# Performance work log

Measured on AMD Instinct MI355X. Metric: run time of the kernel, lower is better.

## Reference

```python
import jax, jax.numpy as jnp
import numpy as np

N_NODES = 100000
N_EDGES = 1600000
D = 128
N_LAYERS = 3
BN_EPS = 1e-5
NORM_EPS = 1e-12


def setup_inputs() -> dict:
    key = jax.random.key(0)
    ks = jax.random.split(key, 4)
    x = jax.random.normal(ks[0], (N_NODES, D), dtype=jnp.float32)
    edge_index = jax.random.randint(ks[1], (2, N_EDGES), 0, N_NODES, dtype=jnp.int32)
    W1 = jax.random.normal(ks[2], (N_LAYERS, D, D), dtype=jnp.float32) * (1.0 / np.sqrt(D))
    W2 = jax.random.normal(ks[3], (N_LAYERS, D, D), dtype=jnp.float32) * (1.0 / np.sqrt(D))
    return {
        "x": x,
        "edge_index": edge_index,
        "W1": W1,
        "b1": jnp.zeros((N_LAYERS, D), jnp.float32),
        "g1": jnp.ones((N_LAYERS, D), jnp.float32),
        "be1": jnp.zeros((N_LAYERS, D), jnp.float32),
        "W2": W2,
        "b2": jnp.zeros((N_LAYERS, D), jnp.float32),
        "g_out": jnp.ones((N_LAYERS - 1, D), jnp.float32),
        "b_out": jnp.zeros((N_LAYERS - 1, D), jnp.float32),
    }


def _batchnorm(h, gamma, beta):
    # BatchNorm1d in training mode: biased batch statistics over nodes.
    mu = jnp.mean(h, axis=0)
    var = jnp.var(h, axis=0)
    return (h - mu) * jax.lax.rsqrt(var + BN_EPS) * gamma + beta


def reference(x, edge_index, W1, b1, g1, be1, W2, b2, g_out, b_out):
    src, dst = edge_index[0], edge_index[1]
    h = x
    for i in range(N_LAYERS):
        # GINConv, eps=0: (1+eps)*x + sum of neighbor messages (scatter-add)
        agg = jax.ops.segment_sum(h[src], dst, num_segments=N_NODES)
        h = h + agg
        # inner MLP: Linear -> BN -> ReLU -> Linear
        h = h @ W1[i] + b1[i]
        h = jax.nn.relu(_batchnorm(h, g1[i], be1[i]))
        h = h @ W2[i] + b2[i]
        if i < N_LAYERS - 1:
            h = jax.nn.relu(_batchnorm(h, g_out[i], b_out[i]))
    # F.normalize(p=2, dim=-1) clamps the norm at 1e-12
    norm = jnp.linalg.norm(h, axis=-1, keepdims=True)
    return h / jnp.maximum(norm, NORM_EPS)
```

## Files before the change

kernel.cpp:

```cpp
#include <hip/hip_runtime.h>

#define M_NODES 100000
#define PADM 100032
#define DIM 128
#define N_EDGES_TOT 1600000
#define NBKT 256
#define NPB 391
#define BKT_CAP 8192
#define ECHUNK 4096
#define INVN 1e-5f
#define NREP 8

typedef unsigned int uint;
typedef unsigned short ushort;
typedef __attribute__((ext_vector_type(8))) short bf16x8;
typedef __attribute__((ext_vector_type(4))) float f32x4;

__device__ __forceinline__ float bflo(uint u) { return __uint_as_float(u << 16); }
__device__ __forceinline__ float bfhi(uint u) { return __uint_as_float(u & 0xffff0000u); }
__device__ __forceinline__ float bf2f(ushort h) { return __uint_as_float(((uint)h) << 16); }
__device__ __forceinline__ ushort f2bf(float f) {
    uint u = __float_as_uint(f);
    return (ushort)((u + 0x7fffu + ((u >> 16) & 1u)) >> 16);
}

__global__ void k_cvt(const float* __restrict__ x, ushort* __restrict__ xb,
                      int n4) {
    int i = blockIdx.x * 256 + threadIdx.x;
    if (i >= n4) return;
    float4 v = ((const float4*)x)[i];
    uint2 r;
    r.x = (uint)f2bf(v.x) | ((uint)f2bf(v.y) << 16);
    r.y = (uint)f2bf(v.z) | ((uint)f2bf(v.w) << 16);
    ((uint2*)xb)[i] = r;
}

__global__ void k_wprep(const float* __restrict__ W1,
                        const float* __restrict__ W2, ushort* __restrict__ Wh,
                        ushort* __restrict__ Wl, float* __restrict__ st,
                        int nSt) {
    int i = blockIdx.x * 256 + threadIdx.x;
    if (i < nSt) st[i] = 0.f;
    if (i >= 6 * 16384) return;
    int l = i >> 14;
    int r = i & 16383;
    int n = r >> 7, k = r & 127;
    const float* W = (l < 3) ? (W1 + l * 16384) : (W2 + (l - 3) * 16384);
    float w = W[k * 128 + n];
    ushort h = f2bf(w);
    Wh[i] = h;
    Wl[i] = f2bf(w - bf2f(h));
}

__global__ void k_bnr(ushort* __restrict__ B0,
                      const float* __restrict__ bnstats,
                      const float* __restrict__ gamma,
                      const float* __restrict__ beta, int n4) {
    __shared__ float coef[256];
    int t = threadIdx.x;
    if (t < 128) {
        float s0 = 0.f, q0 = 0.f;
#pragma unroll
        for (int r = 0; r < NREP; ++r) {
            s0 += bnstats[r * 256 + t];
            q0 += bnstats[r * 256 + 128 + t];
        }
        float mu = s0 * INVN;
        float var = q0 * INVN - mu * mu;
        float s = gamma[t] * rsqrtf(var + 1e-5f);
        coef[t] = s;
        coef[128 + t] = beta[t] - mu * s;
    }
    __syncthreads();
    for (int i = blockIdx.x * 256 + t; i < n4; i += gridDim.x * 256) {
        uint4 v = ((const uint4*)B0)[i];
        int c0 = (i & 15) * 8;
        uint u[4] = {v.x, v.y, v.z, v.w};
        uint o[4];
#pragma unroll
        for (int e = 0; e < 4; ++e) {
            float v0 = fmaxf(fmaf(bflo(u[e]), coef[c0 + 2 * e], coef[128 + c0 + 2 * e]), 0.f);
            float v1 = fmaxf(fmaf(bfhi(u[e]), coef[c0 + 2 * e + 1], coef[128 + c0 + 2 * e + 1]), 0.f);
            o[e] = (uint)f2bf(v0) | ((uint)f2bf(v1) << 16);
        }
        ((uint4*)B0)[i] = make_uint4(o[0], o[1], o[2], o[3]);
    }
}

__global__ void k_bhist(const int* __restrict__ dst, int* __restrict__ cntM,
                        int nE, int nChunks) {
    __shared__ int h[NBKT];
    const int chunk = blockIdx.x, t = threadIdx.x;
    h[t] = 0;
    __syncthreads();
    const int e0 = chunk * ECHUNK;
#pragma unroll
    for (int k = 0; k < 16; ++k) {
        int e = e0 + k * 256 + t;
        if (e < nE) atomicAdd(&h[dst[e] / NPB], 1);
    }
    __syncthreads();
    cntM[t * nChunks + chunk] = h[t];
}

__global__ void k_scanA(int* __restrict__ cnt, int* __restrict__ bsum, int n) {
    __shared__ int s[256];
    int t = threadIdx.x, i = blockIdx.x * 256 + t;
    int v = (i < n) ? cnt[i] : 0;
    s[t] = v;
    __syncthreads();
#pragma unroll
    for (int o = 1; o < 256; o <<= 1) {
        int a = (t >= o) ? s[t - o] : 0;
        __syncthreads();
        s[t] += a;
        __syncthreads();
    }
    if (i < n) cnt[i] = s[t] - v;
    if (t == 255) bsum[blockIdx.x] = s[255];
}

__global__ void k_scanB(int* bsum, int nB) {
    __shared__ int s[1024];
    int t = threadIdx.x;
    int v = (t < nB) ? bsum[t] : 0;
    s[t] = v;
    __syncthreads();
#pragma unroll
    for (int o = 1; o < 1024; o <<= 1) {
        int a = (t >= o) ? s[t - o] : 0;
        __syncthreads();
        s[t] += a;
        __syncthreads();
    }
    if (t < nB) bsum[t] = s[t] - v;
}

__global__ void k_scanC(int* __restrict__ excl, const int* __restrict__ bsum) {
    int i = blockIdx.x * 256 + threadIdx.x;
    excl[i] += bsum[blockIdx.x];
}

__global__ void k_pairs(const int* __restrict__ src, const int* __restrict__ dst,
                        const int* __restrict__ exclM, uint* __restrict__ pairs,
                        int nE, int nChunks) {
    __shared__ int base[NBKT];
    const int chunk = blockIdx.x, t = threadIdx.x;
    base[t] = exclM[t * nChunks + chunk];
    __syncthreads();
    const int e0 = chunk * ECHUNK;
#pragma unroll
    for (int k = 0; k < 16; ++k) {
        int e = e0 + k * 256 + t;
        if (e < nE) {
            int d = dst[e];
            int bkt = d / NPB;
            int pos = atomicAdd(&base[bkt], 1);
            pairs[pos] = ((uint)(d - bkt * NPB) << 17) | (uint)src[e];
        }
    }
}

__global__ void k_csrD(const uint* __restrict__ pairs,
                       const int* __restrict__ exclM, int nChunks,
                       int* __restrict__ rowptr, int* __restrict__ srcs,
                       int nE) {
    __shared__ int cnt[512];
    __shared__ int scn[512];
    __shared__ int sl[BKT_CAP];
    const int b = blockIdx.x, t = threadIdx.x;
    const int base = exclM[b * nChunks];
    const int next = (b == NBKT - 1) ? nE : exclM[(b + 1) * nChunks];
    const int count = next - base;
    const int nodeBase = b * NPB;
    const int nNodes = min(NPB, M_NODES - nodeBase);
    cnt[t] = 0;
    cnt[t + 256] = 0;
    __syncthreads();
    for (int i = t; i < count; i += 256)
        atomicAdd(&cnt[pairs[base + i] >> 17], 1);
    __syncthreads();
    scn[t] = cnt[t];
    scn[t + 256] = cnt[t + 256];
    __syncthreads();
#pragma unroll
    for (int o = 1; o < 512; o <<= 1) {
        int a0 = (t >= o) ? scn[t - o] : 0;
        int a1 = scn[t + 256 - o];
        __syncthreads();
        scn[t] += a0;
        scn[t + 256] += a1;
        __syncthreads();
    }
    int o0 = scn[t] - cnt[t];
    int o1 = scn[t + 256] - cnt[t + 256];
    __syncthreads();
    cnt[t] = o0;
    cnt[t + 256] = o1;
    if (t < nNodes) rowptr[nodeBase + t] = base + o0;
    if (t + 256 < nNodes) rowptr[nodeBase + t + 256] = base + o1;
    if (b == 0 && t == 0) rowptr[M_NODES] = nE;
    __syncthreads();
    const bool inLds = (count <= BKT_CAP);
    for (int i = t; i < count; i += 256) {
        uint p = pairs[base + i];
        int pos = atomicAdd(&cnt[p >> 17], 1);
        int sv = (int)(p & 0x1FFFFu);
        if (inLds) sl[pos] = sv;
        else srcs[base + pos] = sv;
    }
    __syncthreads();
    if (inLds)
        for (int i = t; i < count; i += 256) srcs[base + i] = sl[i];
}

__global__ void k_gather(const ushort* __restrict__ h,
                         const int* __restrict__ rowptr,
                         const int* __restrict__ srcs,
                         ushort* __restrict__ AGh, ushort* __restrict__ AGl,
                         int M) {
    int t = threadIdx.x;
    int node = blockIdx.x * 8 + (t >> 5);
    if (node >= M) return;
    int c = (t & 31) * 4;
    int beg = rowptr[node];
    int end = rowptr[node + 1];

    uint2 v = *(const uint2*)(h + (size_t)node * DIM + c);
    float a0 = bflo(v.x), a1 = bfhi(v.x), a2 = bflo(v.y), a3 = bfhi(v.y);
    float b0 = 0.f, b1 = 0.f, b2 = 0.f, b3 = 0.f;

    int j = beg;
    for (; j + 8 <= end; j += 8) {
        int s[8];
#pragma unroll
        for (int k = 0; k < 8; ++k) s[k] = srcs[j + k];
        uint2 g[8];
#pragma unroll
        for (int k = 0; k < 8; ++k)
            g[k] = *(const uint2*)(h + (size_t)s[k] * DIM + c);
#pragma unroll
        for (int k = 0; k < 8; k += 2) {
            a0 += bflo(g[k].x); a1 += bfhi(g[k].x);
            a2 += bflo(g[k].y); a3 += bfhi(g[k].y);
            b0 += bflo(g[k + 1].x); b1 += bfhi(g[k + 1].x);
            b2 += bflo(g[k + 1].y); b3 += bfhi(g[k + 1].y);
        }
    }
    for (; j + 4 <= end; j += 4) {
        int s0 = srcs[j], s1 = srcs[j + 1], s2 = srcs[j + 2], s3 = srcs[j + 3];
        uint2 g0 = *(const uint2*)(h + (size_t)s0 * DIM + c);
        uint2 g1 = *(const uint2*)(h + (size_t)s1 * DIM + c);
        uint2 g2 = *(const uint2*)(h + (size_t)s2 * DIM + c);
        uint2 g3 = *(const uint2*)(h + (size_t)s3 * DIM + c);
        a0 += bflo(g0.x); a1 += bfhi(g0.x); a2 += bflo(g0.y); a3 += bfhi(g0.y);
        b0 += bflo(g1.x); b1 += bfhi(g1.x); b2 += bflo(g1.y); b3 += bfhi(g1.y);
        a0 += bflo(g2.x); a1 += bfhi(g2.x); a2 += bflo(g2.y); a3 += bfhi(g2.y);
        b0 += bflo(g3.x); b1 += bfhi(g3.x); b2 += bflo(g3.y); b3 += bfhi(g3.y);
    }
    for (; j < end; ++j) {
        int s = srcs[j];
        uint2 g = *(const uint2*)(h + (size_t)s * DIM + c);
        a0 += bflo(g.x); a1 += bfhi(g.x); a2 += bflo(g.y); a3 += bfhi(g.y);
    }
    float s0 = a0 + b0, s1 = a1 + b1, s2 = a2 + b2, s3 = a3 + b3;
    ushort h0 = f2bf(s0), h1 = f2bf(s1), h2 = f2bf(s2), h3 = f2bf(s3);
    ushort l0 = f2bf(s0 - bf2f(h0)), l1 = f2bf(s1 - bf2f(h1));
    ushort l2 = f2bf(s2 - bf2f(h2)), l3 = f2bf(s3 - bf2f(h3));
    uint2 hp, lp;
    hp.x = (uint)h0 | ((uint)h1 << 16);
    hp.y = (uint)h2 | ((uint)h3 << 16);
    lp.x = (uint)l0 | ((uint)l1 << 16);
    lp.y = (uint)l2 | ((uint)l3 << 16);
    size_t ix = (size_t)node * DIM + c;
    *(uint2*)(AGh + ix) = hp;
    *(uint2*)(AGl + ix) = lp;
}

__global__ void __launch_bounds__(256, 4) k_gemmA(
    ushort* __restrict__ Ah, const ushort* __restrict__ Al,
    const ushort* __restrict__ Wh, const ushort* __restrict__ Wl,
    const float* __restrict__ bias, float* __restrict__ statSlot, int M) {
    __shared__ ushort lds[16384];
    const int t = threadIdx.x;
    const int w = t >> 6, lane = t & 63, rq = lane >> 4, rc = lane & 15;
    const int row0 = blockIdx.x * 64;

    bf16x8 wh[4][2], wl[4][2];
#pragma unroll
    for (int kc = 0; kc < 4; ++kc)
#pragma unroll
        for (int jj = 0; jj < 2; ++jj) {
            size_t off = (size_t)(w * 32 + jj * 16 + rc) * DIM + kc * 32 + rq * 8;
            wh[kc][jj] = *(const bf16x8*)(Wh + off);
            wl[kc][jj] = *(const bf16x8*)(Wl + off);
        }

#pragma unroll
    for (int i = 0; i < 8; ++i) {
        int idx = t + i * 256;
        int pl = idx >> 10;
        int r = (idx >> 4) & 63;
        int cb = idx & 15;
        const ushort* p = pl ? Al : Ah;
        uint4 v = *(const uint4*)(p + (size_t)(row0 + r) * DIM + cb * 8);
        *(uint4*)((char*)lds + pl * 16384 + r * 256 +
                  ((cb * 16) ^ ((r & 15) << 4))) = v;
    }
    __syncthreads();

    f32x4 acc[4][2];
#pragma unroll
    for (int i = 0; i < 4; ++i)
#pragma unroll
        for (int jj = 0; jj < 2; ++jj) acc[i][jj] = (f32x4){0.f, 0.f, 0.f, 0.f};

#pragma unroll
    for (int kc = 0; kc < 4; ++kc) {
        const int kb = kc * 64 + rq * 16;
#pragma unroll
        for (int i = 0; i < 4; ++i) {
            int lr = i * 16 + rc;
            int so = lr * 256 + (kb ^ ((lr & 15) << 4));
            bf16x8 ah = *(const bf16x8*)((char*)lds + so);
            bf16x8 al = *(const bf16x8*)((char*)lds + 16384 + so);
#pragma unroll
            for (int jj = 0; jj < 2; ++jj) {
                acc[i][jj] = __builtin_amdgcn_mfma_f32_16x16x32_bf16(ah, wh[kc][jj], acc[i][jj], 0, 0, 0);
                acc[i][jj] = __builtin_amdgcn_mfma_f32_16x16x32_bf16(al, wh[kc][jj], acc[i][jj], 0, 0, 0);
                acc[i][jj] = __builtin_amdgcn_mfma_f32_16x16x32_bf16(ah, wl[kc][jj], acc[i][jj], 0, 0, 0);
            }
        }
    }

    float bc[2] = {bias[w * 32 + rc], bias[w * 32 + 16 + rc]};
    float csum[2] = {0.f, 0.f}, csq[2] = {0.f, 0.f};

    __syncthreads();
#pragma unroll
    for (int i = 0; i < 4; ++i)
#pragma unroll
        for (int r = 0; r < 4; ++r) {
            int lrow = i * 16 + rq * 4 + r;
            bool live = (row0 + lrow) < M;
#pragma unroll
            for (int jj = 0; jj < 2; ++jj) {
                float o = acc[i][jj][r] + bc[jj];
                int off = lrow * 256 +
                          (((w * 32 + jj * 16 + rc) * 2) ^ ((lrow & 15) << 4));
                *(ushort*)((char*)lds + off) = f2bf(o);
                if (live) { csum[jj] += o; csq[jj] += o * o; }
            }
        }
    __syncthreads();
    {
        int lrow = w * 16 + (lane & 15);
        int kq = lane >> 4;
        ushort* dH = Ah + (size_t)row0 * DIM;
#pragma unroll
        for (int kc = 0; kc < 4; ++kc) {
            int off = lrow * 256 + ((kc * 64 + kq * 16) ^ ((lrow & 15) << 4));
            uint4 H = *(uint4*)((char*)lds + off);
            size_t go = ((size_t)(w * 4 + kc) * 64 + lane) * 8;
            *(uint4*)(dH + go) = H;
        }
    }
#pragma unroll
    for (int jj = 0; jj < 2; ++jj) {
        csum[jj] += __shfl_xor(csum[jj], 16);
        csum[jj] += __shfl_xor(csum[jj], 32);
        csq[jj] += __shfl_xor(csq[jj], 16);
        csq[jj] += __shfl_xor(csq[jj], 32);
    }
    float* slot = statSlot + (blockIdx.x & (NREP - 1)) * 256;
    if (lane < 16) {
        atomicAdd(slot + w * 32 + rc, csum[0]);
        atomicAdd(slot + w * 32 + 16 + rc, csum[1]);
        atomicAdd(slot + 128 + w * 32 + rc, csq[0]);
        atomicAdd(slot + 128 + w * 32 + 16 + rc, csq[1]);
    }
}

__global__ void __launch_bounds__(256, 4) k_gemmB(
    const ushort* __restrict__ Ch,
    const ushort* __restrict__ Wh, const ushort* __restrict__ Wl,
    const float* __restrict__ bias, const float* __restrict__ bnstats,
    const float* __restrict__ gamma, const float* __restrict__ beta,
    ushort* __restrict__ Cb, float* __restrict__ outF,
    float* __restrict__ statSlot, int M) {
    __shared__ char smem[16384];
    const int t = threadIdx.x;
    const int w = t >> 6, lane = t & 63, rq = lane >> 4, rc = lane & 15;
    const int row0 = blockIdx.x * 64;

    bf16x8 wh[4][2], wl[4][2];
#pragma unroll
    for (int kc = 0; kc < 4; ++kc)
#pragma unroll
        for (int jj = 0; jj < 2; ++jj) {
            size_t off = (size_t)(w * 32 + jj * 16 + rc) * DIM + kc * 32 + rq * 8;
            wh[kc][jj] = *(const bf16x8*)(Wh + off);
            wl[kc][jj] = *(const bf16x8*)(Wl + off);
        }

    float* coef = (float*)smem;
    if (t < 128) {
        float s0 = 0.f, q0 = 0.f;
#pragma unroll
        for (int r = 0; r < NREP; ++r) {
            s0 += bnstats[r * 256 + t];
            q0 += bnstats[r * 256 + 128 + t];
        }
        float mu = s0 * INVN;
        float var = q0 * INVN - mu * mu;
        float s = gamma[t] * rsqrtf(var + 1e-5f);
        coef[t] = s;
        coef[128 + t] = beta[t] - mu * s;
    }
    __syncthreads();

    const ushort* pH = Ch + (size_t)row0 * DIM;
    const int kq8 = (lane >> 4) * 8;

    f32x4 acc[4][2];
#pragma unroll
    for (int i = 0; i < 4; ++i)
#pragma unroll
        for (int jj = 0; jj < 2; ++jj) acc[i][jj] = (f32x4){0.f, 0.f, 0.f, 0.f};

#pragma unroll
    for (int kc = 0; kc < 4; ++kc) {
        float sc8[8], sh8[8];
#pragma unroll
        for (int e = 0; e < 8; ++e) {
            sc8[e] = coef[kc * 32 + kq8 + e];
            sh8[e] = coef[128 + kc * 32 + kq8 + e];
        }
#pragma unroll
        for (int i = 0; i < 4; ++i) {
            size_t go = ((size_t)(i * 4 + kc) * 64 + lane) * 8;
            uint4 H = *(const uint4*)(pH + go);
            uint hu[4] = {H.x, H.y, H.z, H.w};
            uint oh[4], ol[4];
#pragma unroll
            for (int e = 0; e < 4; ++e) {
                float v0 = bflo(hu[e]);
                float v1 = bfhi(hu[e]);
                v0 = fmaxf(fmaf(v0, sc8[2 * e], sh8[2 * e]), 0.f);
                v1 = fmaxf(fmaf(v1, sc8[2 * e + 1], sh8[2 * e + 1]), 0.f);
                ushort h0 = f2bf(v0), h1 = f2bf(v1);
                oh[e] = (uint)h0 | ((uint)h1 << 16);
                ol[e] = (uint)f2bf(v0 - bf2f(h0)) |
                        ((uint)f2bf(v1 - bf2f(h1)) << 16);
            }
            uint4 AH = make_uint4(oh[0], oh[1], oh[2], oh[3]);
            uint4 AL = make_uint4(ol[0], ol[1], ol[2], ol[3]);
            bf16x8 ah = *(bf16x8*)&AH;
            bf16x8 al = *(bf16x8*)&AL;
#pragma unroll
            for (int jj = 0; jj < 2; ++jj) {
                acc[i][jj] = __builtin_amdgcn_mfma_f32_16x16x32_bf16(ah, wh[kc][jj], acc[i][jj], 0, 0, 0);
                acc[i][jj] = __builtin_amdgcn_mfma_f32_16x16x32_bf16(al, wh[kc][jj], acc[i][jj], 0, 0, 0);
                acc[i][jj] = __builtin_amdgcn_mfma_f32_16x16x32_bf16(ah, wl[kc][jj], acc[i][jj], 0, 0, 0);
            }
        }
    }

    float bc[2] = {bias[w * 32 + rc], bias[w * 32 + 16 + rc]};

    if (outF) {
#pragma unroll
        for (int i = 0; i < 4; ++i)
#pragma unroll
            for (int r = 0; r < 4; ++r)
#pragma unroll
                for (int jj = 0; jj < 2; ++jj) acc[i][jj][r] += bc[jj];
        __syncthreads();
        float* nr = (float*)smem;
#pragma unroll
        for (int i = 0; i < 4; ++i)
#pragma unroll
            for (int r = 0; r < 4; ++r) {
                float ss = acc[i][0][r] * acc[i][0][r] + acc[i][1][r] * acc[i][1][r];
                ss += __shfl_xor(ss, 1);
                ss += __shfl_xor(ss, 2);
                ss += __shfl_xor(ss, 4);
                ss += __shfl_xor(ss, 8);
                if (rc == 0) nr[(i * 16 + rq * 4 + r) * 4 + w] = ss;
            }
        __syncthreads();
#pragma unroll
        for (int i = 0; i < 4; ++i)
#pragma unroll
            for (int r = 0; r < 4; ++r) {
                int lrow = i * 16 + rq * 4 + r;
                float4 q = *(const float4*)(nr + lrow * 4);
                float inv = 1.f / fmaxf(sqrtf(q.x + q.y + q.z + q.w), 1e-12f);
                int row = row0 + lrow;
                if (row < M) {
                    outF[(size_t)row * DIM + w * 32 + rc] = acc[i][0][r] * inv;
                    outF[(size_t)row * DIM + w * 32 + 16 + rc] = acc[i][1][r] * inv;
                }
            }
        return;
    }

    float csum[2] = {0.f, 0.f}, csq[2] = {0.f, 0.f};
    __syncthreads();
#pragma unroll
    for (int i = 0; i < 4; ++i)
#pragma unroll
        for (int r = 0; r < 4; ++r) {
            int lrow = i * 16 + rq * 4 + r;
            bool live = (row0 + lrow) < M;
#pragma unroll
            for (int jj = 0; jj < 2; ++jj) {
                float o = acc[i][jj][r] + bc[jj];
                int off = lrow * 256 +
                          (((w * 32 + jj * 16 + rc) * 2) ^ ((lrow & 15) << 4));
                *(ushort*)(smem + off) = f2bf(o);
                if (live) { csum[jj] += o; csq[jj] += o * o; }
            }
        }
    __syncthreads();
#pragma unroll
    for (int it = 0; it < 4; ++it) {
        int idx = t + it * 256;
        int row = idx >> 4, cb = idx & 15;
        int grow = row0 + row;
        if (grow < M) {
            uint4 v = *(uint4*)(smem + row * 256 + ((cb * 16) ^ ((row & 15) << 4)));
            *(uint4*)(Cb + (size_t)grow * DIM + cb * 8) = v;
        }
    }
#pragma unroll
    for (int jj = 0; jj < 2; ++jj) {
        csum[jj] += __shfl_xor(csum[jj], 16);
        csum[jj] += __shfl_xor(csum[jj], 32);
        csq[jj] += __shfl_xor(csq[jj], 16);
        csq[jj] += __shfl_xor(csq[jj], 32);
    }
    float* slot = statSlot + (blockIdx.x & (NREP - 1)) * 256;
    if (lane < 16) {
        atomicAdd(slot + w * 32 + rc, csum[0]);
        atomicAdd(slot + w * 32 + 16 + rc, csum[1]);
        atomicAdd(slot + 128 + w * 32 + rc, csq[0]);
        atomicAdd(slot + 128 + w * 32 + 16 + rc, csq[1]);
    }
}

extern "C" void kernel_launch(void* const* d_in, const int* in_sizes, int n_in,
                              void* d_out, int out_size, void* d_ws,
                              size_t ws_size, hipStream_t stream) {
    const float* x = (const float*)d_in[0];
    const int* ei = (const int*)d_in[1];
    const float* W1 = (const float*)d_in[2];
    const float* b1 = (const float*)d_in[3];
    const float* g1 = (const float*)d_in[4];
    const float* be1 = (const float*)d_in[5];
    const float* W2 = (const float*)d_in[6];
    const float* b2 = (const float*)d_in[7];
    const float* g_out = (const float*)d_in[8];
    const float* b_out = (const float*)d_in[9];
    float* out = (float*)d_out;

    const int M = M_NODES;
    const int E = N_EDGES_TOT;
    const size_t NM = (size_t)M * DIM;
    const size_t PM = (size_t)PADM * DIM;
    const int nChunks = (E + ECHUNK - 1) / ECHUNK;
    const int nMat = NBKT * nChunks;
    const int SLOT = 256 * NREP;

    ushort* AGh = (ushort*)d_ws;
    ushort* AGl = AGh + PM;
    ushort* B0 = AGl + PM;
    ushort* Wh = B0 + NM;
    ushort* Wl = Wh + 6 * 16384;
    float* st = (float*)(Wl + 6 * 16384);
    float* stA0 = st;
    float* stA1 = st + SLOT;
    float* stA2 = st + 2 * SLOT;
    float* stB0 = st + 3 * SLOT;
    float* stB1 = st + 4 * SLOT;
    uint* pairs = (uint*)(st + 5 * SLOT);
    int* rowptr = (int*)(pairs + E);
    int* cntM = rowptr + (M + 2);
    int* bsum = cntM + nMat;
    int* srcs = bsum + 1024;

    const int* src = ei;
    const int* dst = ei + E;

    const int gemmGrid = PADM / 64;
    const int gathGrid = (M + 7) / 8;
    const int n4 = (int)(NM / 8);

    k_bhist<<<nChunks, 256, 0, stream>>>(dst, cntM, E, nChunks);
    k_scanA<<<(nMat + 255) / 256, 256, 0, stream>>>(cntM, bsum, nMat);
    k_scanB<<<1, 1024, 0, stream>>>(bsum, (nMat + 255) / 256);
    k_scanC<<<(nMat + 255) / 256, 256, 0, stream>>>(cntM, bsum);
    k_pairs<<<nChunks, 256, 0, stream>>>(src, dst, cntM, pairs, E, nChunks);
    k_csrD<<<NBKT, 256, 0, stream>>>(pairs, cntM, nChunks, rowptr, srcs, E);

    k_cvt<<<(int)((NM / 4 + 255) / 256), 256, 0, stream>>>(x, B0, (int)(NM / 4));
    k_wprep<<<(6 * 16384 + 255) / 256, 256, 0, stream>>>(W1, W2, Wh, Wl, st, 5 * SLOT);

    k_gather<<<gathGrid, 256, 0, stream>>>(B0, rowptr, srcs, AGh, AGl, M);
    k_gemmA<<<gemmGrid, 256, 0, stream>>>(AGh, AGl, Wh, Wl, b1, stA0, M);
    k_gemmB<<<gemmGrid, 256, 0, stream>>>(AGh, Wh + 3 * 16384, Wl + 3 * 16384,
                                          b2, stA0, g1, be1, B0, nullptr, stB0, M);
    k_bnr<<<2048, 256, 0, stream>>>(B0, stB0, g_out, b_out, n4);

    k_gather<<<gathGrid, 256, 0, stream>>>(B0, rowptr, srcs, AGh, AGl, M);
    k_gemmA<<<gemmGrid, 256, 0, stream>>>(AGh, AGl, Wh + 16384, Wl + 16384,
                                          b1 + 128, stA1, M);
    k_gemmB<<<gemmGrid, 256, 0, stream>>>(AGh, Wh + 4 * 16384, Wl + 4 * 16384,
                                          b2 + 128, stA1, g1 + 128, be1 + 128,
                                          B0, nullptr, stB1, M);
    k_bnr<<<2048, 256, 0, stream>>>(B0, stB1, g_out + 128, b_out + 128, n4);

    k_gather<<<gathGrid, 256, 0, stream>>>(B0, rowptr, srcs, AGh, AGl, M);
    k_gemmA<<<gemmGrid, 256, 0, stream>>>(AGh, AGl, Wh + 2 * 16384, Wl + 2 * 16384,
                                          b1 + 256, stA2, M);
    k_gemmB<<<gemmGrid, 256, 0, stream>>>(AGh, Wh + 5 * 16384, Wl + 5 * 16384,
                                          b2 + 256, stA2, g1 + 256, be1 + 256,
                                          nullptr, out, nullptr, M);
}
```

Before: 458.6 us.

## Fuse outer BatchNorm+ReLU into neighbor gather and use direct global-to-LDS loads

Removes the standalone k_bnr pass. Each gather block now builds the BN scale/shift coefficients in shared memory and applies affine+ReLU to every gathered neighbor row and the self row. This saves a full read/write pass over the node features twice per forward, at the cost of extra FMA/max work on every gathered element (about 16x more applications than before). Separately, gemmA's tile load now uses global_load_lds with a pre-swizzled source column to skip the register round-trip. The 4-wide remainder loop in gather is also dropped.

```diff
diff --git a/kernel.cpp b/kernel.cpp
--- a/kernel.cpp
+++ b/kernel.cpp
@@ -52,41 +52,6 @@
     Wl[i] = f2bf(w - bf2f(h));
 }
 
-__global__ void k_bnr(ushort* __restrict__ B0,
-                      const float* __restrict__ bnstats,
-                      const float* __restrict__ gamma,
-                      const float* __restrict__ beta, int n4) {
-    __shared__ float coef[256];
-    int t = threadIdx.x;
-    if (t < 128) {
-        float s0 = 0.f, q0 = 0.f;
-#pragma unroll
-        for (int r = 0; r < NREP; ++r) {
-            s0 += bnstats[r * 256 + t];
-            q0 += bnstats[r * 256 + 128 + t];
-        }
-        float mu = s0 * INVN;
-        float var = q0 * INVN - mu * mu;
-        float s = gamma[t] * rsqrtf(var + 1e-5f);
-        coef[t] = s;
-        coef[128 + t] = beta[t] - mu * s;
-    }
-    __syncthreads();
-    for (int i = blockIdx.x * 256 + t; i < n4; i += gridDim.x * 256) {
-        uint4 v = ((const uint4*)B0)[i];
-        int c0 = (i & 15) * 8;
-        uint u[4] = {v.x, v.y, v.z, v.w};
-        uint o[4];
-#pragma unroll
-        for (int e = 0; e < 4; ++e) {
-            float v0 = fmaxf(fmaf(bflo(u[e]), coef[c0 + 2 * e], coef[128 + c0 + 2 * e]), 0.f);
-            float v1 = fmaxf(fmaf(bfhi(u[e]), coef[c0 + 2 * e + 1], coef[128 + c0 + 2 * e + 1]), 0.f);
-            o[e] = (uint)f2bf(v0) | ((uint)f2bf(v1) << 16);
-        }
-        ((uint4*)B0)[i] = make_uint4(o[0], o[1], o[2], o[3]);
-    }
-}
-
 __global__ void k_bhist(const int* __restrict__ dst, int* __restrict__ cntM,
                         int nE, int nChunks) {
     __shared__ int h[NBKT];
@@ -217,17 +182,53 @@
 __global__ void k_gather(const ushort* __restrict__ h,
                          const int* __restrict__ rowptr,
                          const int* __restrict__ srcs,
+                         const float* __restrict__ bnstats,
+                         const float* __restrict__ gamma,
+                         const float* __restrict__ beta,
                          ushort* __restrict__ AGh, ushort* __restrict__ AGl,
                          int M) {
+    __shared__ float coef[256];
     int t = threadIdx.x;
+    const bool bn = (bnstats != nullptr);
+    if (bn) {
+        if (t < 128) {
+            float s0 = 0.f, q0 = 0.f;
+#pragma unroll
+            for (int r = 0; r < NREP; ++r) {
+                s0 += bnstats[r * 256 + t];
+                q0 += bnstats[r * 256 + 128 + t];
+            }
+            float mu = s0 * INVN;
+            float var = q0 * INVN - mu * mu;
+            float s = gamma[t] * rsqrtf(var + 1e-5f);
+            coef[t] = s;
+            coef[128 + t] = beta[t] - mu * s;
+        }
+        __syncthreads();
+    }
     int node = blockIdx.x * 8 + (t >> 5);
     if (node >= M) return;
     int c = (t & 31) * 4;
+    float sc0 = 1.f, sc1 = 1.f, sc2 = 1.f, sc3 = 1.f;
+    float sh0 = 0.f, sh1 = 0.f, sh2 = 0.f, sh3 = 0.f;
+    if (bn) {
+        sc0 = coef[c]; sc1 = coef[c + 1]; sc2 = coef[c + 2]; sc3 = coef[c + 3];
+        sh0 = coef[128 + c]; sh1 = coef[129 + c];
+        sh2 = coef[130 + c]; sh3 = coef[131 + c];
+    }
     int beg = rowptr[node];
     int end = rowptr[node + 1];
 
     uint2 v = *(const uint2*)(h + (size_t)node * DIM + c);
-    float a0 = bflo(v.x), a1 = bfhi(v.x), a2 = bflo(v.y), a3 = bfhi(v.y);
+    float a0, a1, a2, a3;
+    if (bn) {
+        a0 = fmaxf(fmaf(bflo(v.x), sc0, sh0), 0.f);
+        a1 = fmaxf(fmaf(bfhi(v.x), sc1, sh1), 0.f);
+        a2 = fmaxf(fmaf(bflo(v.y), sc2, sh2), 0.f);
+        a3 = fmaxf(fmaf(bfhi(v.y), sc3, sh3), 0.f);
+    } else {
+        a0 = bflo(v.x); a1 = bfhi(v.x); a2 = bflo(v.y); a3 = bfhi(v.y);
+    }
     float b0 = 0.f, b1 = 0.f, b2 = 0.f, b3 = 0.f;
 
     int j = beg;
@@ -239,29 +240,39 @@
 #pragma unroll
         for (int k = 0; k < 8; ++k)
             g[k] = *(const uint2*)(h + (size_t)s[k] * DIM + c);
-#pragma unroll
-        for (int k = 0; k < 8; k += 2) {
-            a0 += bflo(g[k].x); a1 += bfhi(g[k].x);
-            a2 += bflo(g[k].y); a3 += bfhi(g[k].y);
-            b0 += bflo(g[k + 1].x); b1 += bfhi(g[k + 1].x);
-            b2 += bflo(g[k + 1].y); b3 += bfhi(g[k + 1].y);
-        }
-    }
-    for (; j + 4 <= end; j += 4) {
-        int s0 = srcs[j], s1 = srcs[j + 1], s2 = srcs[j + 2], s3 = srcs[j + 3];
-        uint2 g0 = *(const uint2*)(h + (size_t)s0 * DIM + c);
-        uint2 g1 = *(const uint2*)(h + (size_t)s1 * DIM + c);
-        uint2 g2 = *(const uint2*)(h + (size_t)s2 * DIM + c);
-        uint2 g3 = *(const uint2*)(h + (size_t)s3 * DIM + c);
-        a0 += bflo(g0.x); a1 += bfhi(g0.x); a2 += bflo(g0.y); a3 += bfhi(g0.y);
-        b0 += bflo(g1.x); b1 += bfhi(g1.x); b2 += bflo(g1.y); b3 += bfhi(g1.y);
-        a0 += bflo(g2.x); a1 += bfhi(g2.x); a2 += bflo(g2.y); a3 += bfhi(g2.y);
-        b0 += bflo(g3.x); b1 += bfhi(g3.x); b2 += bflo(g3.y); b3 += bfhi(g3.y);
+        if (bn) {
+#pragma unroll
+            for (int k = 0; k < 8; k += 2) {
+                a0 += fmaxf(fmaf(bflo(g[k].x), sc0, sh0), 0.f);
+                a1 += fmaxf(fmaf(bfhi(g[k].x), sc1, sh1), 0.f);
+                a2 += fmaxf(fmaf(bflo(g[k].y), sc2, sh2), 0.f);
+                a3 += fmaxf(fmaf(bfhi(g[k].y), sc3, sh3), 0.f);
+                b0 += fmaxf(fmaf(bflo(g[k + 1].x), sc0, sh0), 0.f);
+                b1 += fmaxf(fmaf(bfhi(g[k + 1].x), sc1, sh1), 0.f);
+                b2 += fmaxf(fmaf(bflo(g[k + 1].y), sc2, sh2), 0.f);
+                b3 += fmaxf(fmaf(bfhi(g[k + 1].y), sc3, sh3), 0.f);
+            }
+        } else {
+#pragma unroll
+            for (int k = 0; k < 8; k += 2) {
+                a0 += bflo(g[k].x); a1 += bfhi(g[k].x);
+                a2 += bflo(g[k].y); a3 += bfhi(g[k].y);
+                b0 += bflo(g[k + 1].x); b1 += bfhi(g[k + 1].x);
+                b2 += bflo(g[k + 1].y); b3 += bfhi(g[k + 1].y);
+            }
+        }
     }
     for (; j < end; ++j) {
         int s = srcs[j];
         uint2 g = *(const uint2*)(h + (size_t)s * DIM + c);
-        a0 += bflo(g.x); a1 += bfhi(g.x); a2 += bflo(g.y); a3 += bfhi(g.y);
+        if (bn) {
+            a0 += fmaxf(fmaf(bflo(g.x), sc0, sh0), 0.f);
+            a1 += fmaxf(fmaf(bfhi(g.x), sc1, sh1), 0.f);
+            a2 += fmaxf(fmaf(bflo(g.y), sc2, sh2), 0.f);
+            a3 += fmaxf(fmaf(bfhi(g.y), sc3, sh3), 0.f);
+        } else {
+            a0 += bflo(g.x); a1 += bfhi(g.x); a2 += bflo(g.y); a3 += bfhi(g.y);
+        }
     }
     float s0 = a0 + b0, s1 = a1 + b1, s2 = a2 + b2, s3 = a3 + b3;
     ushort h0 = f2bf(s0), h1 = f2bf(s1), h2 = f2bf(s2), h3 = f2bf(s3);
@@ -302,10 +313,13 @@
         int pl = idx >> 10;
         int r = (idx >> 4) & 63;
         int cb = idx & 15;
+        int cbs = cb ^ (r & 15);
         const ushort* p = pl ? Al : Ah;
-        uint4 v = *(const uint4*)(p + (size_t)(row0 + r) * DIM + cb * 8);
-        *(uint4*)((char*)lds + pl * 16384 + r * 256 +
-                  ((cb * 16) ^ ((r & 15) << 4))) = v;
+        const ushort* g = p + (size_t)(row0 + r) * DIM + cbs * 8;
+        __builtin_amdgcn_global_load_lds(
+            (const __attribute__((address_space(1))) void*)g,
+            (__attribute__((address_space(3))) void*)((char*)lds + idx * 16),
+            16, 0, 0);
     }
     __syncthreads();
 
@@ -594,7 +608,6 @@
 
     const int gemmGrid = PADM / 64;
     const int gathGrid = (M + 7) / 8;
-    const int n4 = (int)(NM / 8);
 
     k_bhist<<<nChunks, 256, 0, stream>>>(dst, cntM, E, nChunks);
     k_scanA<<<(nMat + 255) / 256, 256, 0, stream>>>(cntM, bsum, nMat);
@@ -606,21 +619,22 @@
     k_cvt<<<(int)((NM / 4 + 255) / 256), 256, 0, stream>>>(x, B0, (int)(NM / 4));
     k_wprep<<<(6 * 16384 + 255) / 256, 256, 0, stream>>>(W1, W2, Wh, Wl, st, 5 * SLOT);
 
-    k_gather<<<gathGrid, 256, 0, stream>>>(B0, rowptr, srcs, AGh, AGl, M);
+    k_gather<<<gathGrid, 256, 0, stream>>>(B0, rowptr, srcs, nullptr, nullptr,
+                                           nullptr, AGh, AGl, M);
     k_gemmA<<<gemmGrid, 256, 0, stream>>>(AGh, AGl, Wh, Wl, b1, stA0, M);
     k_gemmB<<<gemmGrid, 256, 0, stream>>>(AGh, Wh + 3 * 16384, Wl + 3 * 16384,
                                           b2, stA0, g1, be1, B0, nullptr, stB0, M);
-    k_bnr<<<2048, 256, 0, stream>>>(B0, stB0, g_out, b_out, n4);
-
-    k_gather<<<gathGrid, 256, 0, stream>>>(B0, rowptr, srcs, AGh, AGl, M);
+
+    k_gather<<<gathGrid, 256, 0, stream>>>(B0, rowptr, srcs, stB0, g_out, b_out,
+                                           AGh, AGl, M);
     k_gemmA<<<gemmGrid, 256, 0, stream>>>(AGh, AGl, Wh + 16384, Wl + 16384,
                                           b1 + 128, stA1, M);
     k_gemmB<<<gemmGrid, 256, 0, stream>>>(AGh, Wh + 4 * 16384, Wl + 4 * 16384,
                                           b2 + 128, stA1, g1 + 128, be1 + 128,
                                           B0, nullptr, stB1, M);
-    k_bnr<<<2048, 256, 0, stream>>>(B0, stB1, g_out + 128, b_out + 128, n4);
-
-    k_gather<<<gathGrid, 256, 0, stream>>>(B0, rowptr, srcs, AGh, AGl, M);
+
+    k_gather<<<gathGrid, 256, 0, stream>>>(B0, rowptr, srcs, stB1, g_out + 128,
+                                           b_out + 128, AGh, AGl, M);
     k_gemmA<<<gemmGrid, 256, 0, stream>>>(AGh, AGl, Wh + 2 * 16384, Wl + 2 * 16384,
                                           b1 + 256, stA2, M);
     k_gemmB<<<gemmGrid, 256, 0, stream>>>(AGh, Wh + 5 * 16384, Wl + 5 * 16384,
```

Measured after the change: 472.0 us. 1.03x slower.

## Fuse neighbor gather into first GEMM kernel via LDS staging

Applied to the files above, without the earlier changes.

The separate gather kernel is merged into the first GEMM of each layer. Each 64-row block accumulates its neighbor sums directly into swizzled LDS as hi/lo bf16 planes, so the AGh/AGl round trip through global memory goes away. Weight fragments are now loaded per k-chunk instead of all up front, which cuts register use so launch bounds can rise to 5 blocks. The cost is that the latency-bound gather now runs inside a GEMM block with fewer resident threads per node, which may lower memory-level parallelism.

```diff
diff --git a/kernel.cpp b/kernel.cpp
--- a/kernel.cpp
+++ b/kernel.cpp
@@ -214,109 +214,97 @@
         for (int i = t; i < count; i += 256) srcs[base + i] = sl[i];
 }
 
-__global__ void k_gather(const ushort* __restrict__ h,
-                         const int* __restrict__ rowptr,
-                         const int* __restrict__ srcs,
-                         ushort* __restrict__ AGh, ushort* __restrict__ AGl,
-                         int M) {
-    int t = threadIdx.x;
-    int node = blockIdx.x * 8 + (t >> 5);
-    if (node >= M) return;
-    int c = (t & 31) * 4;
-    int beg = rowptr[node];
-    int end = rowptr[node + 1];
-
-    uint2 v = *(const uint2*)(h + (size_t)node * DIM + c);
-    float a0 = bflo(v.x), a1 = bfhi(v.x), a2 = bflo(v.y), a3 = bfhi(v.y);
-    float b0 = 0.f, b1 = 0.f, b2 = 0.f, b3 = 0.f;
-
-    int j = beg;
-    for (; j + 8 <= end; j += 8) {
-        int s[8];
-#pragma unroll
-        for (int k = 0; k < 8; ++k) s[k] = srcs[j + k];
-        uint2 g[8];
-#pragma unroll
-        for (int k = 0; k < 8; ++k)
-            g[k] = *(const uint2*)(h + (size_t)s[k] * DIM + c);
-#pragma unroll
-        for (int k = 0; k < 8; k += 2) {
-            a0 += bflo(g[k].x); a1 += bfhi(g[k].x);
-            a2 += bflo(g[k].y); a3 += bfhi(g[k].y);
-            b0 += bflo(g[k + 1].x); b1 += bfhi(g[k + 1].x);
-            b2 += bflo(g[k + 1].y); b3 += bfhi(g[k + 1].y);
-        }
-    }
-    for (; j + 4 <= end; j += 4) {
-        int s0 = srcs[j], s1 = srcs[j + 1], s2 = srcs[j + 2], s3 = srcs[j + 3];
-        uint2 g0 = *(const uint2*)(h + (size_t)s0 * DIM + c);
-        uint2 g1 = *(const uint2*)(h + (size_t)s1 * DIM + c);
-        uint2 g2 = *(const uint2*)(h + (size_t)s2 * DIM + c);
-        uint2 g3 = *(const uint2*)(h + (size_t)s3 * DIM + c);
-        a0 += bflo(g0.x); a1 += bfhi(g0.x); a2 += bflo(g0.y); a3 += bfhi(g0.y);
-        b0 += bflo(g1.x); b1 += bfhi(g1.x); b2 += bflo(g1.y); b3 += bfhi(g1.y);
-        a0 += bflo(g2.x); a1 += bfhi(g2.x); a2 += bflo(g2.y); a3 += bfhi(g2.y);
-        b0 += bflo(g3.x); b1 += bfhi(g3.x); b2 += bflo(g3.y); b3 += bfhi(g3.y);
-    }
-    for (; j < end; ++j) {
-        int s = srcs[j];
-        uint2 g = *(const uint2*)(h + (size_t)s * DIM + c);
-        a0 += bflo(g.x); a1 += bfhi(g.x); a2 += bflo(g.y); a3 += bfhi(g.y);
-    }
-    float s0 = a0 + b0, s1 = a1 + b1, s2 = a2 + b2, s3 = a3 + b3;
-    ushort h0 = f2bf(s0), h1 = f2bf(s1), h2 = f2bf(s2), h3 = f2bf(s3);
-    ushort l0 = f2bf(s0 - bf2f(h0)), l1 = f2bf(s1 - bf2f(h1));
-    ushort l2 = f2bf(s2 - bf2f(h2)), l3 = f2bf(s3 - bf2f(h3));
-    uint2 hp, lp;
-    hp.x = (uint)h0 | ((uint)h1 << 16);
-    hp.y = (uint)h2 | ((uint)h3 << 16);
-    lp.x = (uint)l0 | ((uint)l1 << 16);
-    lp.y = (uint)l2 | ((uint)l3 << 16);
-    size_t ix = (size_t)node * DIM + c;
-    *(uint2*)(AGh + ix) = hp;
-    *(uint2*)(AGl + ix) = lp;
-}
-
-__global__ void __launch_bounds__(256, 4) k_gemmA(
-    ushort* __restrict__ Ah, const ushort* __restrict__ Al,
-    const ushort* __restrict__ Wh, const ushort* __restrict__ Wl,
-    const float* __restrict__ bias, float* __restrict__ statSlot, int M) {
+__global__ void __launch_bounds__(256, 5) k_gg(
+    const ushort* __restrict__ h, const int* __restrict__ rowptr,
+    const int* __restrict__ srcs, const ushort* __restrict__ Wh,
+    const ushort* __restrict__ Wl, const float* __restrict__ bias,
+    ushort* __restrict__ Ch, float* __restrict__ statSlot, int M) {
     __shared__ ushort lds[16384];
     const int t = threadIdx.x;
+    const int row0 = blockIdx.x * 64;
+
+    {
+        const int g = t >> 5;
+        const int L = t & 31;
+        const int c = L * 4;
+        for (int n = 0; n < 8; ++n) {
+            int lr = g * 8 + n;
+            int node = row0 + lr;
+            float a0 = 0.f, a1 = 0.f, a2 = 0.f, a3 = 0.f;
+            float b0 = 0.f, b1 = 0.f, b2 = 0.f, b3 = 0.f;
+            if (node < M) {
+                uint2 v = *(const uint2*)(h + (size_t)node * DIM + c);
+                a0 = bflo(v.x); a1 = bfhi(v.x); a2 = bflo(v.y); a3 = bfhi(v.y);
+                int beg = rowptr[node];
+                int end = rowptr[node + 1];
+                int j = beg;
+                for (; j + 8 <= end; j += 8) {
+                    int s[8];
+#pragma unroll
+                    for (int k = 0; k < 8; ++k) s[k] = srcs[j + k];
+                    uint2 gg[8];
+#pragma unroll
+                    for (int k = 0; k < 8; ++k)
+                        gg[k] = *(const uint2*)(h + (size_t)s[k] * DIM + c);
+#pragma unroll
+                    for (int k = 0; k < 8; k += 2) {
+                        a0 += bflo(gg[k].x); a1 += bfhi(gg[k].x);
+                        a2 += bflo(gg[k].y); a3 += bfhi(gg[k].y);
+                        b0 += bflo(gg[k + 1].x); b1 += bfhi(gg[k + 1].x);
+                        b2 += bflo(gg[k + 1].y); b3 += bfhi(gg[k + 1].y);
+                    }
+                }
+                for (; j + 4 <= end; j += 4) {
+                    int s0 = srcs[j], s1 = srcs[j + 1];
+                    int s2 = srcs[j + 2], s3 = srcs[j + 3];
+                    uint2 g0 = *(const uint2*)(h + (size_t)s0 * DIM + c);
+                    uint2 g1 = *(const uint2*)(h + (size_t)s1 * DIM + c);
+                    uint2 g2 = *(const uint2*)(h + (size_t)s2 * DIM + c);
+                    uint2 g3 = *(const uint2*)(h + (size_t)s3 * DIM + c);
+                    a0 += bflo(g0.x); a1 += bfhi(g0.x); a2 += bflo(g0.y); a3 += bfhi(g0.y);
+                    b0 += bflo(g1.x); b1 += bfhi(g1.x); b2 += bflo(g1.y); b3 += bfhi(g1.y);
+                    a0 += bflo(g2.x); a1 += bfhi(g2.x); a2 += bflo(g2.y); a3 += bfhi(g2.y);
+                    b0 += bflo(g3.x); b1 += bfhi(g3.x); b2 += bflo(g3.y); b3 += bfhi(g3.y);
+                }
+                for (; j < end; ++j) {
+                    int s = srcs[j];
+                    uint2 gg = *(const uint2*)(h + (size_t)s * DIM + c);
+                    a0 += bflo(gg.x); a1 += bfhi(gg.x);
+                    a2 += bflo(gg.y); a3 += bfhi(gg.y);
+                }
+            }
+            float s0 = a0 + b0, s1 = a1 + b1, s2 = a2 + b2, s3 = a3 + b3;
+            ushort h0 = f2bf(s0), h1 = f2bf(s1), h2 = f2bf(s2), h3 = f2bf(s3);
+            ushort l0 = f2bf(s0 - bf2f(h0)), l1 = f2bf(s1 - bf2f(h1));
+            ushort l2 = f2bf(s2 - bf2f(h2)), l3 = f2bf(s3 - bf2f(h3));
+            uint2 hp, lp;
+            hp.x = (uint)h0 | ((uint)h1 << 16);
+            hp.y = (uint)h2 | ((uint)h3 << 16);
+            lp.x = (uint)l0 | ((uint)l1 << 16);
+            lp.y = (uint)l2 | ((uint)l3 << 16);
+            int off = lr * 256 + ((((L >> 1) * 16) ^ ((lr & 15) << 4))) + (L & 1) * 8;
+            *(uint2*)((char*)lds + off) = hp;
+            *(uint2*)((char*)lds + 16384 + off) = lp;
+        }
+    }
+    __syncthreads();
+
     const int w = t >> 6, lane = t & 63, rq = lane >> 4, rc = lane & 15;
-    const int row0 = blockIdx.x * 64;
-
-    bf16x8 wh[4][2], wl[4][2];
-#pragma unroll
-    for (int kc = 0; kc < 4; ++kc)
+    f32x4 acc[4][2];
+#pragma unroll
+    for (int i = 0; i < 4; ++i)
+#pragma unroll
+        for (int jj = 0; jj < 2; ++jj) acc[i][jj] = (f32x4){0.f, 0.f, 0.f, 0.f};
+
+#pragma unroll
+    for (int kc = 0; kc < 4; ++kc) {
+        bf16x8 bh[2], bl[2];
 #pragma unroll
         for (int jj = 0; jj < 2; ++jj) {
             size_t off = (size_t)(w * 32 + jj * 16 + rc) * DIM + kc * 32 + rq * 8;
-            wh[kc][jj] = *(const bf16x8*)(Wh + off);
-            wl[kc][jj] = *(const bf16x8*)(Wl + off);
-        }
-
-#pragma unroll
-    for (int i = 0; i < 8; ++i) {
-        int idx = t + i * 256;
-        int pl = idx >> 10;
-        int r = (idx >> 4) & 63;
-        int cb = idx & 15;
-        const ushort* p = pl ? Al : Ah;
-        uint4 v = *(const uint4*)(p + (size_t)(row0 + r) * DIM + cb * 8);
-        *(uint4*)((char*)lds + pl * 16384 + r * 256 +
-                  ((cb * 16) ^ ((r & 15) << 4))) = v;
-    }
-    __syncthreads();
-
-    f32x4 acc[4][2];
-#pragma unroll
-    for (int i = 0; i < 4; ++i)
-#pragma unroll
-        for (int jj = 0; jj < 2; ++jj) acc[i][jj] = (f32x4){0.f, 0.f, 0.f, 0.f};
-
-#pragma unroll
-    for (int kc = 0; kc < 4; ++kc) {
+            bh[jj] = *(const bf16x8*)(Wh + off);
+            bl[jj] = *(const bf16x8*)(Wl + off);
+        }
         const int kb = kc * 64 + rq * 16;
 #pragma unroll
         for (int i = 0; i < 4; ++i) {
@@ -326,9 +314,9 @@
             bf16x8 al = *(const bf16x8*)((char*)lds + 16384 + so);
 #pragma unroll
             for (int jj = 0; jj < 2; ++jj) {
-                acc[i][jj] = __builtin_amdgcn_mfma_f32_16x16x32_bf16(ah, wh[kc][jj], acc[i][jj], 0, 0, 0);
-                acc[i][jj] = __builtin_amdgcn_mfma_f32_16x16x32_bf16(al, wh[kc][jj], acc[i][jj], 0, 0, 0);
-                acc[i][jj] = __builtin_amdgcn_mfma_f32_16x16x32_bf16(ah, wl[kc][jj], acc[i][jj], 0, 0, 0);
+                acc[i][jj] = __builtin_amdgcn_mfma_f32_16x16x32_bf16(ah, bh[jj], acc[i][jj], 0, 0, 0);
+                acc[i][jj] = __builtin_amdgcn_mfma_f32_16x16x32_bf16(al, bh[jj], acc[i][jj], 0, 0, 0);
+                acc[i][jj] = __builtin_amdgcn_mfma_f32_16x16x32_bf16(ah, bl[jj], acc[i][jj], 0, 0, 0);
             }
         }
     }
@@ -356,7 +344,7 @@
     {
         int lrow = w * 16 + (lane & 15);
         int kq = lane >> 4;
-        ushort* dH = Ah + (size_t)row0 * DIM;
+        ushort* dH = Ch + (size_t)row0 * DIM;
 #pragma unroll
         for (int kc = 0; kc < 4; ++kc) {
             int off = lrow * 256 + ((kc * 64 + kq * 16) ^ ((lrow & 15) << 4));
@@ -572,9 +560,8 @@
     const int nMat = NBKT * nChunks;
     const int SLOT = 256 * NREP;
 
-    ushort* AGh = (ushort*)d_ws;
-    ushort* AGl = AGh + PM;
-    ushort* B0 = AGl + PM;
+    ushort* Ch = (ushort*)d_ws;
+    ushort* B0 = Ch + PM;
     ushort* Wh = B0 + NM;
     ushort* Wl = Wh + 6 * 16384;
     float* st = (float*)(Wl + 6 * 16384);
@@ -593,7 +580,6 @@
     const int* dst = ei + E;
 
     const int gemmGrid = PADM / 64;
-    const int gathGrid = (M + 7) / 8;
     const int n4 = (int)(NM / 8);
 
     k_bhist<<<nChunks, 256, 0, stream>>>(dst, cntM, E, nChunks);
@@ -606,24 +592,21 @@
     k_cvt<<<(int)((NM / 4 + 255) / 256), 256, 0, stream>>>(x, B0, (int)(NM / 4));
     k_wprep<<<(6 * 16384 + 255) / 256, 256, 0, stream>>>(W1, W2, Wh, Wl, st, 5 * SLOT);
 
-    k_gather<<<gathGrid, 256, 0, stream>>>(B0, rowptr, srcs, AGh, AGl, M);
-    k_gemmA<<<gemmGrid, 256, 0, stream>>>(AGh, AGl, Wh, Wl, b1, stA0, M);
-    k_gemmB<<<gemmGrid, 256, 0, stream>>>(AGh, Wh + 3 * 16384, Wl + 3 * 16384,
+    k_gg<<<gemmGrid, 256, 0, stream>>>(B0, rowptr, srcs, Wh, Wl, b1, Ch, stA0, M);
+    k_gemmB<<<gemmGrid, 256, 0, stream>>>(Ch, Wh + 3 * 16384, Wl + 3 * 16384,
                                           b2, stA0, g1, be1, B0, nullptr, stB0, M);
     k_bnr<<<2048, 256, 0, stream>>>(B0, stB0, g_out, b_out, n4);
 
-    k_gather<<<gathGrid, 256, 0, stream>>>(B0, rowptr, srcs, AGh, AGl, M);
-    k_gemmA<<<gemmGrid, 256, 0, stream>>>(AGh, AGl, Wh + 16384, Wl + 16384,
-                                          b1 + 128, stA1, M);
-    k_gemmB<<<gemmGrid, 256, 0, stream>>>(AGh, Wh + 4 * 16384, Wl + 4 * 16384,
+    k_gg<<<gemmGrid, 256, 0, stream>>>(B0, rowptr, srcs, Wh + 16384, Wl + 16384,
+                                       b1 + 128, Ch, stA1, M);
+    k_gemmB<<<gemmGrid, 256, 0, stream>>>(Ch, Wh + 4 * 16384, Wl + 4 * 16384,
                                           b2 + 128, stA1, g1 + 128, be1 + 128,
                                           B0, nullptr, stB1, M);
     k_bnr<<<2048, 256, 0, stream>>>(B0, stB1, g_out + 128, b_out + 128, n4);
 
-    k_gather<<<gathGrid, 256, 0, stream>>>(B0, rowptr, srcs, AGh, AGl, M);
-    k_gemmA<<<gemmGrid, 256, 0, stream>>>(AGh, AGl, Wh + 2 * 16384, Wl + 2 * 16384,
-                                          b1 + 256, stA2, M);
-    k_gemmB<<<gemmGrid, 256, 0, stream>>>(AGh, Wh + 5 * 16384, Wl + 5 * 16384,
+    k_gg<<<gemmGrid, 256, 0, stream>>>(B0, rowptr, srcs, Wh + 2 * 16384,
+                                       Wl + 2 * 16384, b1 + 256, Ch, stA2, M);
+    k_gemmB<<<gemmGrid, 256, 0, stream>>>(Ch, Wh + 5 * 16384, Wl + 5 * 16384,
                                           b2 + 256, stA2, g1 + 256, be1 + 256,
                                           nullptr, out, nullptr, M);
 }
```

New measurement: 482.8 us. 5.3% more time.
